# Kernel optimization log

Measured on AMD Instinct MI355X. Metric: run time of the kernel, lower is better.

Reference implementation:

```python
import jax, jax.numpy as jnp
import numpy as np

T, B, H, NC, NM = 200, 256, 512, 3, 64  # time, batch, hidden, nb_classes, nb_measures


def setup_inputs() -> dict:
    key = jax.random.key(0)
    ks = jax.random.split(key, 12)

    def p(k, *sh):
        return jax.random.normal(k, sh, dtype=jnp.float32) * 0.05

    return dict(
        cat_seq=jax.random.normal(ks[0], (T, B, NC), dtype=jnp.float32),
        val_seq=jax.random.normal(ks[1], (T, B, NM), dtype=jnp.float32),
        # layer 0 RNN cell: input = nb_classes + nb_measures
        W_ih0=p(ks[2], NC + NM, H), W_hh0=p(ks[3], H, H), b0=p(ks[4], H),
        # layer 1 RNN cell
        W_ih1=p(ks[5], H, H), W_hh1=p(ks[6], H, H), b1=p(ks[7], H),
        # hid2category / hid2measures heads
        Wc=p(ks[8], H, NC), bc=p(ks[9], NC),
        Wm=p(ks[10], H, NM), bm=p(ks[11], NM),
    )


def reference(cat_seq, val_seq, W_ih0, W_hh0, b0, W_ih1, W_hh1, b1, Wc, bc, Wm, bm):
    # Eval mode: dropout masks (i_mask, r_mask) are all ones -> no-ops, omitted.
    batch = val_seq.shape[1]
    h0 = jnp.zeros((batch, W_hh0.shape[0]), dtype=val_seq.dtype)
    h1 = jnp.zeros_like(h0)

    def step(carry, xs):
        h0, h1, cat_i, val_i = carry
        cat_next, val_next = xs
        # predict(): concat(cat, val*i_mask) -> stacked tanh RNN cells -> heads
        x = jnp.concatenate([cat_i, val_i], axis=-1)          # [B, NC+NM]
        h0 = jnp.tanh(x @ W_ih0 + h0 @ W_hh0 + b0)            # [B, H]
        h1 = jnp.tanh(h0 @ W_ih1 + h1 @ W_hh1 + b1)           # [B, H]
        o_cat = jax.nn.softmax(h1 @ Wc + bc, axis=-1)         # [B, NC]
        o_val = h1 @ Wm + bm + val_i                          # [B, NM]
        # impute NaNs of the next timestep with model predictions (on-device)
        val_next = jnp.where(jnp.isnan(val_next), o_val, val_next)
        cat_next = jnp.where(jnp.isnan(cat_next), o_cat, cat_next)
        return (h0, h1, cat_next, val_next), o_cat

    carry0 = (h0, h1, cat_seq[0], val_seq[0])
    _, out_cat = jax.lax.scan(step, carry0, (cat_seq[1:], val_seq[1:]))
    return out_cat  # [T-1, B, NC] == torch.stack(out_cat_seq)
```

## Files before the change

### kernel.cpp

```cpp
#include <hip/hip_runtime.h>
#include <math.h>


#define SZ_WCAT0 (579u * 512u)
#define OFF_WCAT0 0u
#define OFF_WCAT1 (OFF_WCAT0 + SZ_WCAT0)
#define SZ_WCAT1 (1024u * 512u)
#define OFF_H0 (OFF_WCAT1 + SZ_WCAT1)
#define SZ_HBUF (256u * 512u)
#define OFF_H1 (OFF_H0 + 2u * SZ_HBUF)
#define OFF_CAT (OFF_H1 + 2u * SZ_HBUF)
#define SZ_CATB (256u * 3u)
#define OFF_VAL (OFF_CAT + 2u * SZ_CATB)
#define SZ_VALB (256u * 64u)

__device__ __forceinline__ bool nanf_bits(float v) {
  return (__float_as_uint(v) & 0x7fffffffu) > 0x7f800000u;
}

__global__ __launch_bounds__(256) void pack_weights(
    const float* __restrict__ Wih0, const float* __restrict__ Whh0,
    const float* __restrict__ Wih1, const float* __restrict__ Whh1,
    float* __restrict__ Wc0, float* __restrict__ Wc1) {
  unsigned idx = blockIdx.x * 256u + threadIdx.x;
  unsigned stride = gridDim.x * 256u;
  for (unsigned i = idx; i < SZ_WCAT0; i += stride) {
    unsigned r = i >> 9, c = i & 511u;
    float v;
    if (r < 64u)       v = Wih0[(3u + r) * 512u + c];
    else if (r < 576u) v = Whh0[(r - 64u) * 512u + c];
    else               v = Wih0[(r - 576u) * 512u + c];
    Wc0[i] = v;
  }
  for (unsigned i = idx; i < SZ_WCAT1; i += stride) {
    unsigned r = i >> 9, c = i & 511u;
    Wc1[i] = (r < 512u) ? Wih1[r * 512u + c] : Whh1[(r - 512u) * 512u + c];
  }
}

__global__ __launch_bounds__(256) void init_state(
    const float* __restrict__ cat_seq, const float* __restrict__ val_seq,
    float* __restrict__ h0a, float* __restrict__ h1a,
    float* __restrict__ cata, float* __restrict__ vala) {
  unsigned idx = blockIdx.x * 256u + threadIdx.x;
  h0a[idx] = 0.f;
  h1a[idx] = 0.f;
  if (idx < SZ_CATB) cata[idx] = cat_seq[idx];
  if (idx < SZ_VALB) vala[idx] = val_seq[idx];
}

template <int PHASE>
__global__ __launch_bounds__(256) void step_gemm(
    const float* __restrict__ a0, const float* __restrict__ a1,
    const float* __restrict__ a2, const float* __restrict__ W,
    const float* __restrict__ bias, float* __restrict__ out) {
  constexpr int KS = (PHASE == 0) ? 592 : 1040;
  __shared__ float As[8 * KS];
  __shared__ float red[2048];
  const int tid = threadIdx.x;
  const int row0 = blockIdx.x * 8;

  if (PHASE == 0) {
    if (tid < 128) {
      int r = tid >> 4, q = tid & 15;
      *(float4*)&As[r * KS + q * 4] = *(const float4*)&a0[(row0 + r) * 64 + q * 4];
    }
    for (int i = tid; i < 1024; i += 256) {
      int r = i >> 7, q = i & 127;
      *(float4*)&As[r * KS + 64 + q * 4] = *(const float4*)&a1[(row0 + r) * 512 + q * 4];
    }
    if (tid < 24) {
      int r = tid / 3, j = tid % 3;
      As[r * KS + 576 + j] = a2[(row0 + r) * 3 + j];
    }
    if (tid < 104) {
      int r = tid / 13, j = tid % 13;
      As[r * KS + 579 + j] = 0.f;
    }
  } else {
    for (int i = tid; i < 1024; i += 256) {
      int r = i >> 7, q = i & 127;
      *(float4*)&As[r * KS + q * 4] = *(const float4*)&a0[(row0 + r) * 512 + q * 4];
    }
    for (int i = tid; i < 1024; i += 256) {
      int r = i >> 7, q = i & 127;
      *(float4*)&As[r * KS + 512 + q * 4] = *(const float4*)&a1[(row0 + r) * 512 + q * 4];
    }
    if (tid < 128) {
      int r = tid >> 4, j = tid & 15;
      As[r * KS + 1024 + j] = 0.f;
    }
  }
  __syncthreads();

  const int kg = tid >> 6, item = tid & 63;
  const int rp = (tid >> 4) & 3, qx = tid & 15;
  const int r0 = 2 * rp, r1 = r0 + 1;
  const int colb = blockIdx.y * 64 + qx * 4;
  const int kq = KS / 4;
  const int ka = kg * kq;
  float acc0[4] = {0, 0, 0, 0}, acc1[4] = {0, 0, 0, 0};
  const float* Wp = W + (size_t)ka * 512 + colb;
  const float* A0p = &As[r0 * KS + ka];
  const float* A1p = &As[r1 * KS + ka];
  for (int k = 0; k < kq; k += 4) {
    float4 A0 = *(const float4*)(A0p + k);
    float4 A1 = *(const float4*)(A1p + k);
    float a0c[4] = {A0.x, A0.y, A0.z, A0.w};
    float a1c[4] = {A1.x, A1.y, A1.z, A1.w};
#pragma unroll
    for (int j = 0; j < 4; ++j) {
      float4 wj = *(const float4*)(Wp + j * 512);
      acc0[0] += a0c[j] * wj.x; acc0[1] += a0c[j] * wj.y;
      acc0[2] += a0c[j] * wj.z; acc0[3] += a0c[j] * wj.w;
      acc1[0] += a1c[j] * wj.x; acc1[1] += a1c[j] * wj.y;
      acc1[2] += a1c[j] * wj.z; acc1[3] += a1c[j] * wj.w;
    }
    Wp += 2048;
  }
#pragma unroll
  for (int a = 0; a < 4; ++a) {
    red[kg * 512 + item * 8 + a] = acc0[a];
    red[kg * 512 + item * 8 + 4 + a] = acc1[a];
  }
  __syncthreads();
  if (tid < 64) {
    float s[8];
#pragma unroll
    for (int a = 0; a < 8; ++a)
      s[a] = red[item * 8 + a] + red[512 + item * 8 + a] +
             red[1024 + item * 8 + a] + red[1536 + item * 8 + a];
    float4 o0, o1;
    o0.x = tanhf(s[0] + bias[colb + 0]);
    o0.y = tanhf(s[1] + bias[colb + 1]);
    o0.z = tanhf(s[2] + bias[colb + 2]);
    o0.w = tanhf(s[3] + bias[colb + 3]);
    o1.x = tanhf(s[4] + bias[colb + 0]);
    o1.y = tanhf(s[5] + bias[colb + 1]);
    o1.z = tanhf(s[6] + bias[colb + 2]);
    o1.w = tanhf(s[7] + bias[colb + 3]);
    *(float4*)&out[(row0 + r0) * 512 + colb] = o0;
    *(float4*)&out[(row0 + r1) * 512 + colb] = o1;
  }
}

__global__ __launch_bounds__(256) void phase_c(
    const float* __restrict__ h1n, const float* __restrict__ valp,
    const float* __restrict__ cat_seq, const float* __restrict__ val_seq,
    const float* __restrict__ Wc, const float* __restrict__ bc,
    const float* __restrict__ Wm, const float* __restrict__ bm,
    float* __restrict__ out, float* __restrict__ catn,
    float* __restrict__ valn, int step) {
  __shared__ float h1s[8 * 512];
  __shared__ float redc[4 * 64 * 8];
  __shared__ float redc2[192];
  __shared__ float catd[24];
  const int tid = threadIdx.x;
  const int row0 = blockIdx.x * 8;
  for (int i = tid; i < 1024; i += 256) {
    int r = i >> 7, q = i & 127;
    *(float4*)&h1s[r * 512 + q * 4] = *(const float4*)&h1n[(row0 + r) * 512 + q * 4];
  }
  __syncthreads();

  const int m = tid & 63, sub = tid >> 6;
  float acc[8] = {0, 0, 0, 0, 0, 0, 0, 0};
  {
    const float* wmp = Wm + (size_t)(sub * 128) * 64 + m;
    const int kb = sub * 128;
    for (int k = 0; k < 128; ++k) {
      float w = wmp[(size_t)k * 64];
#pragma unroll
      for (int r = 0; r < 8; ++r) acc[r] += h1s[r * 512 + kb + k] * w;
    }
  }
#pragma unroll
  for (int r = 0; r < 8; ++r) redc[sub * 512 + m * 8 + r] = acc[r];
  __syncthreads();

  if (tid < 64) {
#pragma unroll
    for (int r = 0; r < 8; ++r) {
      float s = redc[tid * 8 + r] + redc[512 + tid * 8 + r] +
                redc[1024 + tid * 8 + r] + redc[1536 + tid * 8 + r];
      float ov = s + bm[tid] + valp[(row0 + r) * 64 + tid];
      float raw = val_seq[(size_t)(step + 1) * (256 * 64) + (row0 + r) * 64 + tid];
      valn[(row0 + r) * 64 + tid] = nanf_bits(raw) ? ov : raw;
    }
  } else {
    int l = tid - 64;
    int d = l % 24, ks = l / 24;
    int r = d / 3, j = d % 3;
    float a = 0.f;
    const int kb = ks * 64;
    for (int k = 0; k < 64; ++k) a += h1s[r * 512 + kb + k] * Wc[(kb + k) * 3 + j];
    redc2[ks * 24 + d] = a;
  }
  __syncthreads();
  if (tid < 24) {
    float s = bc[tid % 3];
#pragma unroll
    for (int ks = 0; ks < 8; ++ks) s += redc2[ks * 24 + tid];
    catd[tid] = s;
  }
  __syncthreads();
  if (tid < 8) {
    int r = tid;
    float a0 = catd[r * 3 + 0], a1 = catd[r * 3 + 1], a2 = catd[r * 3 + 2];
    float mx = fmaxf(a0, fmaxf(a1, a2));
    float e0 = expf(a0 - mx), e1 = expf(a1 - mx), e2 = expf(a2 - mx);
    float inv = 1.f / (e0 + e1 + e2);
    float p0 = e0 * inv, p1 = e1 * inv, p2 = e2 * inv;
    size_t ob = (size_t)step * (256 * 3) + (size_t)(row0 + r) * 3;
    out[ob + 0] = p0; out[ob + 1] = p1; out[ob + 2] = p2;
    size_t cb = (size_t)(step + 1) * (256 * 3) + (size_t)(row0 + r) * 3;
    float c0 = cat_seq[cb + 0], c1 = cat_seq[cb + 1], c2 = cat_seq[cb + 2];
    catn[(row0 + r) * 3 + 0] = nanf_bits(c0) ? p0 : c0;
    catn[(row0 + r) * 3 + 1] = nanf_bits(c1) ? p1 : c1;
    catn[(row0 + r) * 3 + 2] = nanf_bits(c2) ? p2 : c2;
  }
}

extern "C" void kernel_launch(void* const* d_in, const int* in_sizes, int n_in,
                              void* d_out, int out_size, void* d_ws, size_t ws_size,
                              hipStream_t stream) {
  const float* cat_seq = (const float*)d_in[0];
  const float* val_seq = (const float*)d_in[1];
  const float* Wih0 = (const float*)d_in[2];
  const float* Whh0 = (const float*)d_in[3];
  const float* b0 = (const float*)d_in[4];
  const float* Wih1 = (const float*)d_in[5];
  const float* Whh1 = (const float*)d_in[6];
  const float* b1 = (const float*)d_in[7];
  const float* Wc = (const float*)d_in[8];
  const float* bc = (const float*)d_in[9];
  const float* Wm = (const float*)d_in[10];
  const float* bm = (const float*)d_in[11];
  float* ws = (float*)d_ws;
  float* Wc0 = ws + OFF_WCAT0;
  float* Wc1 = ws + OFF_WCAT1;
  float* h0b[2] = {ws + OFF_H0, ws + OFF_H0 + SZ_HBUF};
  float* h1b[2] = {ws + OFF_H1, ws + OFF_H1 + SZ_HBUF};
  float* catb[2] = {ws + OFF_CAT, ws + OFF_CAT + SZ_CATB};
  float* valb[2] = {ws + OFF_VAL, ws + OFF_VAL + SZ_VALB};
  float* out = (float*)d_out;

  hipLaunchKernelGGL(pack_weights, dim3(2048), dim3(256), 0, stream,
                     Wih0, Whh0, Wih1, Whh1, Wc0, Wc1);
  hipLaunchKernelGGL(init_state, dim3(512), dim3(256), 0, stream,
                     cat_seq, val_seq, h0b[0], h1b[0], catb[0], valb[0]);
  int p = 0;
  for (int i = 0; i < 199; ++i) {
    int q = p ^ 1;
    hipLaunchKernelGGL((step_gemm<0>), dim3(32, 8), dim3(256), 0, stream,
                       valb[p], h0b[p], catb[p], Wc0, b0, h0b[q]);
    hipLaunchKernelGGL((step_gemm<1>), dim3(32, 8), dim3(256), 0, stream,
                       h0b[q], h1b[p], (const float*)nullptr, Wc1, b1, h1b[q]);
    hipLaunchKernelGGL(phase_c, dim3(32), dim3(256), 0, stream,
                       h1b[q], valb[p], cat_seq, val_seq, Wc, bc, Wm, bm,
                       out, catb[q], valb[q], i);
    p = q;
  }
}
```

Measured before the change: 6.875 ms.

## Replace per-step kernel launches with single persistent cooperative kernel using grid syncs

Replaces the 597 separate kernel launches with one cooperative kernel of 256 blocks that loops over all timesteps, separated by grid-wide barriers. The recurrence is restructured so h0 @ Whh0 and h0 @ Wih1 share one phase while h1 @ Whh1 is precomputed into Q1. The small input projection, heads and imputation run on dedicated blocks, and weight packing is removed. This removes launch overhead and inter-kernel gaps, at the cost of grid-sync latency, 512-thread blocks and a different register-tiled GEMM.

```diff
diff --git a/kernel.cpp b/kernel.cpp
--- a/kernel.cpp
+++ b/kernel.cpp
@@ -1,223 +1,224 @@
 #include <hip/hip_runtime.h>
+#include <hip/hip_cooperative_groups.h>
 #include <math.h>
 
-
-#define SZ_WCAT0 (579u * 512u)
-#define OFF_WCAT0 0u
-#define OFF_WCAT1 (OFF_WCAT0 + SZ_WCAT0)
-#define SZ_WCAT1 (1024u * 512u)
-#define OFF_H0 (OFF_WCAT1 + SZ_WCAT1)
-#define SZ_HBUF (256u * 512u)
-#define OFF_H1 (OFF_H0 + 2u * SZ_HBUF)
-#define OFF_CAT (OFF_H1 + 2u * SZ_HBUF)
-#define SZ_CATB (256u * 3u)
-#define OFF_VAL (OFF_CAT + 2u * SZ_CATB)
-#define SZ_VALB (256u * 64u)
+namespace cg = cooperative_groups;
+
+
+#define OFF_H1 131072
+#define OFF_Q1 262144
+#define OFF_R0 393216
+#define OFF_VALC 524288
 
 __device__ __forceinline__ bool nanf_bits(float v) {
   return (__float_as_uint(v) & 0x7fffffffu) > 0x7f800000u;
 }
 
-__global__ __launch_bounds__(256) void pack_weights(
+__device__ __forceinline__ void mk44(const float4 av[4], const float4 wv[4],
+                                     float acc[4][4]) {
+#pragma unroll
+  for (int ri = 0; ri < 4; ++ri) {
+    const float ax = av[ri].x, ay = av[ri].y, az = av[ri].z, aw = av[ri].w;
+    acc[ri][0] += ax * wv[0].x + ay * wv[1].x + az * wv[2].x + aw * wv[3].x;
+    acc[ri][1] += ax * wv[0].y + ay * wv[1].y + az * wv[2].y + aw * wv[3].y;
+    acc[ri][2] += ax * wv[0].z + ay * wv[1].z + az * wv[2].z + aw * wv[3].z;
+    acc[ri][3] += ax * wv[0].w + ay * wv[1].w + az * wv[2].w + aw * wv[3].w;
+  }
+}
+
+__device__ __forceinline__ void gemm64(const float* __restrict__ Ap,
+                                       const float* __restrict__ Wp,
+                                       float acc[4][4]) {
+  for (int k = 0; k < 64; k += 4) {
+    float4 av[4], wv[4];
+    av[0] = *(const float4*)(Ap + k);
+    av[1] = *(const float4*)(Ap + 512 + k);
+    av[2] = *(const float4*)(Ap + 1024 + k);
+    av[3] = *(const float4*)(Ap + 1536 + k);
+    wv[0] = *(const float4*)(Wp + (size_t)(k + 0) * 512);
+    wv[1] = *(const float4*)(Wp + (size_t)(k + 1) * 512);
+    wv[2] = *(const float4*)(Wp + (size_t)(k + 2) * 512);
+    wv[3] = *(const float4*)(Wp + (size_t)(k + 3) * 512);
+    mk44(av, wv, acc);
+  }
+}
+
+__global__ __launch_bounds__(512) void rnn_all(
+    const float* __restrict__ cat_seq, const float* __restrict__ val_seq,
     const float* __restrict__ Wih0, const float* __restrict__ Whh0,
-    const float* __restrict__ Wih1, const float* __restrict__ Whh1,
-    float* __restrict__ Wc0, float* __restrict__ Wc1) {
-  unsigned idx = blockIdx.x * 256u + threadIdx.x;
-  unsigned stride = gridDim.x * 256u;
-  for (unsigned i = idx; i < SZ_WCAT0; i += stride) {
-    unsigned r = i >> 9, c = i & 511u;
-    float v;
-    if (r < 64u)       v = Wih0[(3u + r) * 512u + c];
-    else if (r < 576u) v = Whh0[(r - 64u) * 512u + c];
-    else               v = Wih0[(r - 576u) * 512u + c];
-    Wc0[i] = v;
-  }
-  for (unsigned i = idx; i < SZ_WCAT1; i += stride) {
-    unsigned r = i >> 9, c = i & 511u;
-    Wc1[i] = (r < 512u) ? Wih1[r * 512u + c] : Whh1[(r - 512u) * 512u + c];
-  }
-}
-
-__global__ __launch_bounds__(256) void init_state(
-    const float* __restrict__ cat_seq, const float* __restrict__ val_seq,
-    float* __restrict__ h0a, float* __restrict__ h1a,
-    float* __restrict__ cata, float* __restrict__ vala) {
-  unsigned idx = blockIdx.x * 256u + threadIdx.x;
-  h0a[idx] = 0.f;
-  h1a[idx] = 0.f;
-  if (idx < SZ_CATB) cata[idx] = cat_seq[idx];
-  if (idx < SZ_VALB) vala[idx] = val_seq[idx];
-}
-
-template <int PHASE>
-__global__ __launch_bounds__(256) void step_gemm(
-    const float* __restrict__ a0, const float* __restrict__ a1,
-    const float* __restrict__ a2, const float* __restrict__ W,
-    const float* __restrict__ bias, float* __restrict__ out) {
-  constexpr int KS = (PHASE == 0) ? 592 : 1040;
-  __shared__ float As[8 * KS];
-  __shared__ float red[2048];
-  const int tid = threadIdx.x;
-  const int row0 = blockIdx.x * 8;
-
-  if (PHASE == 0) {
-    if (tid < 128) {
-      int r = tid >> 4, q = tid & 15;
-      *(float4*)&As[r * KS + q * 4] = *(const float4*)&a0[(row0 + r) * 64 + q * 4];
+    const float* __restrict__ b0v, const float* __restrict__ Wih1,
+    const float* __restrict__ Whh1, const float* __restrict__ b1v,
+    const float* __restrict__ Wc, const float* __restrict__ bcv,
+    const float* __restrict__ Wm, const float* __restrict__ bmv,
+    float* __restrict__ out, float* __restrict__ ws) {
+  cg::grid_group grid = cg::this_grid();
+  float* h0 = ws;
+  float* h1 = ws + OFF_H1;
+  float* Q1 = ws + OFF_Q1;
+  float* R0 = ws + OFF_R0;
+  float* valc = ws + OFF_VALC;
+  const int w = blockIdx.x, tid = threadIdx.x;
+
+  __shared__ float red[8704];
+  __shared__ float h1s[2][512];
+  __shared__ float xs[2][68];
+  __shared__ float red2[512];
+  __shared__ float redc[6];
+
+  {
+    if (tid < 64) {
+      float v = val_seq[(size_t)w * 64 + tid];
+      valc[(size_t)w * 64 + tid] = v;
+      xs[0][3 + tid] = v;
+    } else if (tid < 67) {
+      xs[0][tid - 64] = cat_seq[(size_t)w * 3 + (tid - 64)];
     }
-    for (int i = tid; i < 1024; i += 256) {
-      int r = i >> 7, q = i & 127;
-      *(float4*)&As[r * KS + 64 + q * 4] = *(const float4*)&a1[(row0 + r) * 512 + q * 4];
+    __syncthreads();
+    float a = b0v[tid];
+    for (int k = 0; k < 67; ++k) a += xs[0][k] * Wih0[(size_t)k * 512 + tid];
+    h0[(size_t)w * 512 + tid] = tanhf(a);
+    Q1[(size_t)w * 512 + tid] = 0.f;
+  }
+  grid.sync();
+
+  for (int i = 0; i < 199; ++i) {
+    {
+      const int g = tid >> 8;
+      const int kq = (tid >> 5) & 7;
+      const int pos = tid & 31;
+      const int r0 = (w >> 5) * 32, c0 = (w & 31) * 16;
+      const int kb = kq * 64;
+      const float* Ap = h0 + (size_t)(r0 + (pos >> 2) * 4) * 512 + kb;
+      const float* Wp = (g ? Whh0 : Wih1) + (size_t)kb * 512 + c0 + (pos & 3) * 4;
+      float acc[4][4] = {};
+      gemm64(Ap, Wp, acc);
+      float* rp = red + (g * 8 + kq) * 544 + pos * 17;
+#pragma unroll
+      for (int ri = 0; ri < 4; ++ri)
+#pragma unroll
+        for (int cj = 0; cj < 4; ++cj) rp[ri * 4 + cj] = acc[ri][cj];
+      __syncthreads();
+      {
+        const int g2 = tid >> 8, t8 = tid & 255;
+        const int opos = t8 >> 3, oe = (t8 * 2) & 15;
+        const int row = r0 + (opos >> 2) * 4 + (oe >> 2);
+        const int col = c0 + (opos & 3) * 4 + (oe & 3);
+        const float* rb = red + g2 * 4352 + opos * 17 + oe;
+        float s0 = 0.f, s1 = 0.f;
+#pragma unroll
+        for (int q = 0; q < 8; ++q) { s0 += rb[q * 544]; s1 += rb[q * 544 + 1]; }
+        if (g2 == 0) {
+          const float2 qv = *(const float2*)(Q1 + (size_t)row * 512 + col);
+          float2 o;
+          o.x = tanhf(s0 + qv.x + b1v[col]);
+          o.y = tanhf(s1 + qv.y + b1v[col + 1]);
+          *(float2*)(h1 + (size_t)row * 512 + col) = o;
+        } else {
+          float2 o = {s0, s1};
+          *(float2*)(R0 + (size_t)row * 512 + col) = o;
+        }
+      }
     }
-    if (tid < 24) {
-      int r = tid / 3, j = tid % 3;
-      As[r * KS + 576 + j] = a2[(row0 + r) * 3 + j];
+    grid.sync();
+    if (w < 128) {
+      const int kq = tid >> 6, pos = tid & 63;
+      const int r0 = (w >> 4) * 32, c0 = (w & 15) * 32;
+      const int kb = kq * 64;
+      const float* Ap = h1 + (size_t)(r0 + (pos >> 3) * 4) * 512 + kb;
+      const float* Wp = Whh1 + (size_t)kb * 512 + c0 + (pos & 7) * 4;
+      float acc[4][4] = {};
+      gemm64(Ap, Wp, acc);
+      float* rp = red + kq * 1088 + pos * 17;
+#pragma unroll
+      for (int ri = 0; ri < 4; ++ri)
+#pragma unroll
+        for (int cj = 0; cj < 4; ++cj) rp[ri * 4 + cj] = acc[ri][cj];
+      __syncthreads();
+      {
+        const int opos = tid >> 3, oe = (tid * 2) & 15;
+        const int row = r0 + (opos >> 3) * 4 + (oe >> 2);
+        const int col = c0 + (opos & 7) * 4 + (oe & 3);
+        const float* rb = red + opos * 17 + oe;
+        float s0 = 0.f, s1 = 0.f;
+#pragma unroll
+        for (int q = 0; q < 8; ++q) { s0 += rb[q * 1088]; s1 += rb[q * 1088 + 1]; }
+        float2 o = {s0, s1};
+        *(float2*)(Q1 + (size_t)row * 512 + col) = o;
+      }
+    } else {
+      const int row0 = (w - 128) * 2;
+      if (tid < 256) {
+        const int r = tid >> 7, q = tid & 127;
+        *(float4*)&h1s[r][q * 4] =
+            *(const float4*)(h1 + (size_t)(row0 + r) * 512 + q * 4);
+      }
+      __syncthreads();
+      {
+        const int m = tid & 63, r = (tid >> 6) & 1, ks = tid >> 7;
+        const float* hp = &h1s[r][ks * 128];
+        const float* wp = Wm + (size_t)(ks * 128) * 64 + m;
+        float a = 0.f;
+        for (int k = 0; k < 128; ++k) a += hp[k] * wp[(size_t)k * 64];
+        red2[(ks * 2 + r) * 64 + m] = a;
+      }
+      __syncthreads();
+      if (tid < 128) {
+        const int m = tid & 63, r = tid >> 6;
+        float s = red2[r * 64 + m] + red2[(2 + r) * 64 + m] +
+                  red2[(4 + r) * 64 + m] + red2[(6 + r) * 64 + m];
+        float ov = s + bmv[m] + valc[(size_t)(row0 + r) * 64 + m];
+        float raw = val_seq[(size_t)(i + 1) * 16384 + (size_t)(row0 + r) * 64 + m];
+        float nv = nanf_bits(raw) ? ov : raw;
+        valc[(size_t)(row0 + r) * 64 + m] = nv;
+        xs[r][3 + m] = nv;
+      } else {
+        const int l = tid - 128;
+        const int d = l >> 6, lane = l & 63;
+        const int r = d / 3, j = d % 3;
+        float a = 0.f;
+        const float* hp = &h1s[r][lane * 8];
+        const float* wp = Wc + (size_t)(lane * 8) * 3 + j;
+#pragma unroll
+        for (int k = 0; k < 8; ++k) a += hp[k] * wp[k * 3];
+        a += __shfl_down(a, 32);
+        a += __shfl_down(a, 16);
+        a += __shfl_down(a, 8);
+        a += __shfl_down(a, 4);
+        a += __shfl_down(a, 2);
+        a += __shfl_down(a, 1);
+        if (lane == 0) redc[d] = a + bcv[j];
+      }
+      __syncthreads();
+      if (tid < 2) {
+        const int r = tid;
+        float l0 = redc[r * 3], l1 = redc[r * 3 + 1], l2 = redc[r * 3 + 2];
+        float mx = fmaxf(l0, fmaxf(l1, l2));
+        float e0 = expf(l0 - mx), e1 = expf(l1 - mx), e2 = expf(l2 - mx);
+        float inv = 1.f / (e0 + e1 + e2);
+        float p0 = e0 * inv, p1 = e1 * inv, p2 = e2 * inv;
+        size_t ob = (size_t)i * 768 + (size_t)(row0 + r) * 3;
+        out[ob] = p0; out[ob + 1] = p1; out[ob + 2] = p2;
+        size_t cb = (size_t)(i + 1) * 768 + (size_t)(row0 + r) * 3;
+        float c0_ = cat_seq[cb], c1_ = cat_seq[cb + 1], c2_ = cat_seq[cb + 2];
+        xs[r][0] = nanf_bits(c0_) ? p0 : c0_;
+        xs[r][1] = nanf_bits(c1_) ? p1 : c1_;
+        xs[r][2] = nanf_bits(c2_) ? p2 : c2_;
+      }
+      __syncthreads();
+      {
+        const int r = tid >> 8, c = tid & 255;
+        float a0 = b0v[c] + R0[(size_t)(row0 + r) * 512 + c];
+        float a1 = b0v[c + 256] + R0[(size_t)(row0 + r) * 512 + c + 256];
+        for (int k = 0; k < 67; ++k) {
+          const float x = xs[r][k];
+          a0 += x * Wih0[(size_t)k * 512 + c];
+          a1 += x * Wih0[(size_t)k * 512 + c + 256];
+        }
+        h0[(size_t)(row0 + r) * 512 + c] = tanhf(a0);
+        h0[(size_t)(row0 + r) * 512 + c + 256] = tanhf(a1);
+      }
     }
-    if (tid < 104) {
-      int r = tid / 13, j = tid % 13;
-      As[r * KS + 579 + j] = 0.f;
-    }
-  } else {
-    for (int i = tid; i < 1024; i += 256) {
-      int r = i >> 7, q = i & 127;
-      *(float4*)&As[r * KS + q * 4] = *(const float4*)&a0[(row0 + r) * 512 + q * 4];
-    }
-    for (int i = tid; i < 1024; i += 256) {
-      int r = i >> 7, q = i & 127;
-      *(float4*)&As[r * KS + 512 + q * 4] = *(const float4*)&a1[(row0 + r) * 512 + q * 4];
-    }
-    if (tid < 128) {
-      int r = tid >> 4, j = tid & 15;
-      As[r * KS + 1024 + j] = 0.f;
-    }
-  }
-  __syncthreads();
-
-  const int kg = tid >> 6, item = tid & 63;
-  const int rp = (tid >> 4) & 3, qx = tid & 15;
-  const int r0 = 2 * rp, r1 = r0 + 1;
-  const int colb = blockIdx.y * 64 + qx * 4;
-  const int kq = KS / 4;
-  const int ka = kg * kq;
-  float acc0[4] = {0, 0, 0, 0}, acc1[4] = {0, 0, 0, 0};
-  const float* Wp = W + (size_t)ka * 512 + colb;
-  const float* A0p = &As[r0 * KS + ka];
-  const float* A1p = &As[r1 * KS + ka];
-  for (int k = 0; k < kq; k += 4) {
-    float4 A0 = *(const float4*)(A0p + k);
-    float4 A1 = *(const float4*)(A1p + k);
-    float a0c[4] = {A0.x, A0.y, A0.z, A0.w};
-    float a1c[4] = {A1.x, A1.y, A1.z, A1.w};
-#pragma unroll
-    for (int j = 0; j < 4; ++j) {
-      float4 wj = *(const float4*)(Wp + j * 512);
-      acc0[0] += a0c[j] * wj.x; acc0[1] += a0c[j] * wj.y;
-      acc0[2] += a0c[j] * wj.z; acc0[3] += a0c[j] * wj.w;
-      acc1[0] += a1c[j] * wj.x; acc1[1] += a1c[j] * wj.y;
-      acc1[2] += a1c[j] * wj.z; acc1[3] += a1c[j] * wj.w;
-    }
-    Wp += 2048;
-  }
-#pragma unroll
-  for (int a = 0; a < 4; ++a) {
-    red[kg * 512 + item * 8 + a] = acc0[a];
-    red[kg * 512 + item * 8 + 4 + a] = acc1[a];
-  }
-  __syncthreads();
-  if (tid < 64) {
-    float s[8];
-#pragma unroll
-    for (int a = 0; a < 8; ++a)
-      s[a] = red[item * 8 + a] + red[512 + item * 8 + a] +
-             red[1024 + item * 8 + a] + red[1536 + item * 8 + a];
-    float4 o0, o1;
-    o0.x = tanhf(s[0] + bias[colb + 0]);
-    o0.y = tanhf(s[1] + bias[colb + 1]);
-    o0.z = tanhf(s[2] + bias[colb + 2]);
-    o0.w = tanhf(s[3] + bias[colb + 3]);
-    o1.x = tanhf(s[4] + bias[colb + 0]);
-    o1.y = tanhf(s[5] + bias[colb + 1]);
-    o1.z = tanhf(s[6] + bias[colb + 2]);
-    o1.w = tanhf(s[7] + bias[colb + 3]);
-    *(float4*)&out[(row0 + r0) * 512 + colb] = o0;
-    *(float4*)&out[(row0 + r1) * 512 + colb] = o1;
-  }
-}
-
-__global__ __launch_bounds__(256) void phase_c(
-    const float* __restrict__ h1n, const float* __restrict__ valp,
-    const float* __restrict__ cat_seq, const float* __restrict__ val_seq,
-    const float* __restrict__ Wc, const float* __restrict__ bc,
-    const float* __restrict__ Wm, const float* __restrict__ bm,
-    float* __restrict__ out, float* __restrict__ catn,
-    float* __restrict__ valn, int step) {
-  __shared__ float h1s[8 * 512];
-  __shared__ float redc[4 * 64 * 8];
-  __shared__ float redc2[192];
-  __shared__ float catd[24];
-  const int tid = threadIdx.x;
-  const int row0 = blockIdx.x * 8;
-  for (int i = tid; i < 1024; i += 256) {
-    int r = i >> 7, q = i & 127;
-    *(float4*)&h1s[r * 512 + q * 4] = *(const float4*)&h1n[(row0 + r) * 512 + q * 4];
-  }
-  __syncthreads();
-
-  const int m = tid & 63, sub = tid >> 6;
-  float acc[8] = {0, 0, 0, 0, 0, 0, 0, 0};
-  {
-    const float* wmp = Wm + (size_t)(sub * 128) * 64 + m;
-    const int kb = sub * 128;
-    for (int k = 0; k < 128; ++k) {
-      float w = wmp[(size_t)k * 64];
-#pragma unroll
-      for (int r = 0; r < 8; ++r) acc[r] += h1s[r * 512 + kb + k] * w;
-    }
-  }
-#pragma unroll
-  for (int r = 0; r < 8; ++r) redc[sub * 512 + m * 8 + r] = acc[r];
-  __syncthreads();
-
-  if (tid < 64) {
-#pragma unroll
-    for (int r = 0; r < 8; ++r) {
-      float s = redc[tid * 8 + r] + redc[512 + tid * 8 + r] +
-                redc[1024 + tid * 8 + r] + redc[1536 + tid * 8 + r];
-      float ov = s + bm[tid] + valp[(row0 + r) * 64 + tid];
-      float raw = val_seq[(size_t)(step + 1) * (256 * 64) + (row0 + r) * 64 + tid];
-      valn[(row0 + r) * 64 + tid] = nanf_bits(raw) ? ov : raw;
-    }
-  } else {
-    int l = tid - 64;
-    int d = l % 24, ks = l / 24;
-    int r = d / 3, j = d % 3;
-    float a = 0.f;
-    const int kb = ks * 64;
-    for (int k = 0; k < 64; ++k) a += h1s[r * 512 + kb + k] * Wc[(kb + k) * 3 + j];
-    redc2[ks * 24 + d] = a;
-  }
-  __syncthreads();
-  if (tid < 24) {
-    float s = bc[tid % 3];
-#pragma unroll
-    for (int ks = 0; ks < 8; ++ks) s += redc2[ks * 24 + tid];
-    catd[tid] = s;
-  }
-  __syncthreads();
-  if (tid < 8) {
-    int r = tid;
-    float a0 = catd[r * 3 + 0], a1 = catd[r * 3 + 1], a2 = catd[r * 3 + 2];
-    float mx = fmaxf(a0, fmaxf(a1, a2));
-    float e0 = expf(a0 - mx), e1 = expf(a1 - mx), e2 = expf(a2 - mx);
-    float inv = 1.f / (e0 + e1 + e2);
-    float p0 = e0 * inv, p1 = e1 * inv, p2 = e2 * inv;
-    size_t ob = (size_t)step * (256 * 3) + (size_t)(row0 + r) * 3;
-    out[ob + 0] = p0; out[ob + 1] = p1; out[ob + 2] = p2;
-    size_t cb = (size_t)(step + 1) * (256 * 3) + (size_t)(row0 + r) * 3;
-    float c0 = cat_seq[cb + 0], c1 = cat_seq[cb + 1], c2 = cat_seq[cb + 2];
-    catn[(row0 + r) * 3 + 0] = nanf_bits(c0) ? p0 : c0;
-    catn[(row0 + r) * 3 + 1] = nanf_bits(c1) ? p1 : c1;
-    catn[(row0 + r) * 3 + 2] = nanf_bits(c2) ? p2 : c2;
+    grid.sync();
   }
 }
 
@@ -236,29 +237,13 @@
   const float* bc = (const float*)d_in[9];
   const float* Wm = (const float*)d_in[10];
   const float* bm = (const float*)d_in[11];
-  float* ws = (float*)d_ws;
-  float* Wc0 = ws + OFF_WCAT0;
-  float* Wc1 = ws + OFF_WCAT1;
-  float* h0b[2] = {ws + OFF_H0, ws + OFF_H0 + SZ_HBUF};
-  float* h1b[2] = {ws + OFF_H1, ws + OFF_H1 + SZ_HBUF};
-  float* catb[2] = {ws + OFF_CAT, ws + OFF_CAT + SZ_CATB};
-  float* valb[2] = {ws + OFF_VAL, ws + OFF_VAL + SZ_VALB};
-  float* out = (float*)d_out;
-
-  hipLaunchKernelGGL(pack_weights, dim3(2048), dim3(256), 0, stream,
-                     Wih0, Whh0, Wih1, Whh1, Wc0, Wc1);
-  hipLaunchKernelGGL(init_state, dim3(512), dim3(256), 0, stream,
-                     cat_seq, val_seq, h0b[0], h1b[0], catb[0], valb[0]);
-  int p = 0;
-  for (int i = 0; i < 199; ++i) {
-    int q = p ^ 1;
-    hipLaunchKernelGGL((step_gemm<0>), dim3(32, 8), dim3(256), 0, stream,
-                       valb[p], h0b[p], catb[p], Wc0, b0, h0b[q]);
-    hipLaunchKernelGGL((step_gemm<1>), dim3(32, 8), dim3(256), 0, stream,
-                       h0b[q], h1b[p], (const float*)nullptr, Wc1, b1, h1b[q]);
-    hipLaunchKernelGGL(phase_c, dim3(32), dim3(256), 0, stream,
-                       h1b[q], valb[p], cat_seq, val_seq, Wc, bc, Wm, bm,
-                       out, catb[q], valb[q], i);
-    p = q;
-  }
-}
+  float* outp = (float*)d_out;
+  float* wsp = (float*)d_ws;
+
+  void* args[] = {(void*)&cat_seq, (void*)&val_seq, (void*)&Wih0, (void*)&Whh0,
+                  (void*)&b0,      (void*)&Wih1,    (void*)&Whh1, (void*)&b1,
+                  (void*)&Wc,      (void*)&bc,      (void*)&Wm,   (void*)&bm,
+                  (void*)&outp,    (void*)&wsp};
+  hipLaunchCooperativeKernel((void*)rnn_all, dim3(256), dim3(512), args, 0,
+                             stream);
+}
```

Result: slower. 27.25 ms (+296.4%).
